# Kernel tuning notes

Hardware: AMD Instinct MI355X
Metric: run time of the kernel (lower is better)

Reference implementation:

```python
import jax, jax.numpy as jnp
import numpy as np
import math

TAU = 3.0
THRESHOLD = 0.25
BETA = 10.0
DT = 1.0


def setup_inputs() -> dict:
    key = jax.random.key(0)
    B, F, L = 64, 512, 1024
    I = jax.random.normal(key, (B, F, L), dtype=jnp.float32)
    return {"I": I}


def reference(I):
    dtype = I.dtype
    alpha = jnp.asarray(math.exp(-DT / TAU), dtype=dtype)
    thr = jnp.asarray(THRESHOLD, dtype=dtype)
    beta = jnp.asarray(BETA, dtype=dtype)

    B, F, L = I.shape
    I_t = jnp.moveaxis(I, -1, 0)  # (L, B, F) for scan over time
    v0 = jnp.zeros((B, F), dtype=dtype)

    def step(v, i_t):
        v_pre = alpha * v + (1 - alpha) * i_t
        z = beta * (v_pre - thr)
        s = (v_pre >= thr).astype(dtype)
        v_new = v_pre * (1 - s)  # threshold-triggered reset
        return v_new, (z, s)

    _, (z_hist, s_hist) = jax.lax.scan(step, v0, I_t)
    # (L, B, F) -> (B, F, L)
    return jnp.moveaxis(z_hist, 0, -1), jnp.moveaxis(s_hist, 0, -1)
```

## Files before the change

kernel.cpp:

```cpp
#include <hip/hip_runtime.h>


constexpr int L_LEN = 1024;

__global__ __launch_bounds__(64) void lif_kernel(
    const float* __restrict__ I, float* __restrict__ Z,
    float* __restrict__ S, int nrows)
{
#pragma clang fp contract(off)
    int row = blockIdx.x * 64 + threadIdx.x;
    if (row >= nrows) return;

    const float alpha = 0.7165313105737893f;
    const float oma   = 1.0f - alpha;
    const float thr   = 0.25f;
    const float beta  = 10.0f;

    const float4* in4 = reinterpret_cast<const float4*>(I) + (size_t)row * (L_LEN / 4);
    float4*       z4  = reinterpret_cast<float4*>(Z)       + (size_t)row * (L_LEN / 4);
    float4*       s4  = reinterpret_cast<float4*>(S)       + (size_t)row * (L_LEN / 4);

    float v = 0.0f;
#pragma unroll 8
    for (int t = 0; t < L_LEN / 4; ++t) {
        float4 x = in4[t];
        float4 zo, so;
        float vp;

        vp = alpha * v + oma * x.x;
        zo.x = beta * (vp - thr);
        so.x = (vp >= thr) ? 1.0f : 0.0f;
        v    = (vp >= thr) ? 0.0f : vp;

        vp = alpha * v + oma * x.y;
        zo.y = beta * (vp - thr);
        so.y = (vp >= thr) ? 1.0f : 0.0f;
        v    = (vp >= thr) ? 0.0f : vp;

        vp = alpha * v + oma * x.z;
        zo.z = beta * (vp - thr);
        so.z = (vp >= thr) ? 1.0f : 0.0f;
        v    = (vp >= thr) ? 0.0f : vp;

        vp = alpha * v + oma * x.w;
        zo.w = beta * (vp - thr);
        so.w = (vp >= thr) ? 1.0f : 0.0f;
        v    = (vp >= thr) ? 0.0f : vp;

        z4[t] = zo;
        s4[t] = so;
    }
}

extern "C" void kernel_launch(void* const* d_in, const int* in_sizes, int n_in,
                              void* d_out, int out_size, void* d_ws, size_t ws_size,
                              hipStream_t stream) {
    const float* I = (const float*)d_in[0];
    int n_elems = in_sizes[0];
    int nrows   = n_elems / L_LEN;

    float* Z = (float*)d_out;
    float* S = (float*)d_out + (size_t)n_elems;

    int block = 64;
    int grid  = (nrows + block - 1) / block;
    lif_kernel<<<grid, block, 0, stream>>>(I, Z, S, nrows);
}
```

Baseline: 424.0 us.

## Split LIF scan into state pass and chunk-parallel output pass

```diff
diff --git a/kernel.cpp b/kernel.cpp
--- a/kernel.cpp
+++ b/kernel.cpp
@@ -1,20 +1,119 @@
 #include <hip/hip_runtime.h>
 
 
-constexpr int L_LEN = 1024;
+constexpr int L_LEN  = 1024;
+constexpr int CHUNK  = 64;
+constexpr int NCHUNK = L_LEN / CHUNK;
 
-__global__ __launch_bounds__(64) void lif_kernel(
+#define ALPHA 0.7165313105737893f
+#define OMA   (1.0f - 0.7165313105737893f)
+#define THR   0.25f
+#define BETA  10.0f
+
+__global__ __launch_bounds__(64) void lif_phase1(
+    const float* __restrict__ I, float* __restrict__ states, int nrows)
+{
+#pragma clang fp contract(off)
+    int row = blockIdx.x * 64 + threadIdx.x;
+    if (row >= nrows) return;
+
+    const float4* in4 = reinterpret_cast<const float4*>(I) + (size_t)row * (L_LEN / 4);
+
+    float st[NCHUNK];
+    float v = 0.0f;
+
+    float4 buf[8];
+#pragma unroll
+    for (int j = 0; j < 8; ++j) buf[j] = in4[j];
+
+    const int nblk = L_LEN / 32;
+    for (int blk = 0; blk < nblk; ++blk) {
+        float4 nxt[8];
+        if (blk + 1 < nblk) {
+#pragma unroll
+            for (int j = 0; j < 8; ++j) nxt[j] = in4[(blk + 1) * 8 + j];
+        } else {
+#pragma unroll
+            for (int j = 0; j < 8; ++j) nxt[j] = make_float4(0.f, 0.f, 0.f, 0.f);
+        }
+
+        if ((blk & 1) == 0) st[blk >> 1] = v;
+
+#pragma unroll
+        for (int j = 0; j < 8; ++j) {
+            float4 x = buf[j];
+            float vp;
+            vp = ALPHA * v + OMA * x.x;  v = (vp >= THR) ? 0.0f : vp;
+            vp = ALPHA * v + OMA * x.y;  v = (vp >= THR) ? 0.0f : vp;
+            vp = ALPHA * v + OMA * x.z;  v = (vp >= THR) ? 0.0f : vp;
+            vp = ALPHA * v + OMA * x.w;  v = (vp >= THR) ? 0.0f : vp;
+        }
+#pragma unroll
+        for (int j = 0; j < 8; ++j) buf[j] = nxt[j];
+    }
+
+    float4* sp = reinterpret_cast<float4*>(states) + (size_t)row * (NCHUNK / 4);
+#pragma unroll
+    for (int c = 0; c < NCHUNK / 4; ++c)
+        sp[c] = make_float4(st[4*c], st[4*c+1], st[4*c+2], st[4*c+3]);
+}
+
+__global__ __launch_bounds__(256) void lif_phase2(
+    const float* __restrict__ I, const float* __restrict__ states,
+    float* __restrict__ Z, float* __restrict__ S, int nthreads)
+{
+#pragma clang fp contract(off)
+    int tid = blockIdx.x * 256 + threadIdx.x;
+    if (tid >= nthreads) return;
+
+    int row = tid >> 4;
+    int c   = tid & 15;
+
+    float v = states[tid];
+
+    size_t base = (size_t)row * (L_LEN / 4) + (size_t)c * (CHUNK / 4);
+    const float4* in4 = reinterpret_cast<const float4*>(I) + base;
+    float4*       z4  = reinterpret_cast<float4*>(Z) + base;
+    float4*       s4  = reinterpret_cast<float4*>(S) + base;
+
+#pragma unroll
+    for (int t = 0; t < CHUNK / 4; ++t) {
+        float4 x = in4[t];
+        float4 zo, so;
+        float vp;
+
+        vp = ALPHA * v + OMA * x.x;
+        zo.x = BETA * (vp - THR);
+        so.x = (vp >= THR) ? 1.0f : 0.0f;
+        v    = (vp >= THR) ? 0.0f : vp;
+
+        vp = ALPHA * v + OMA * x.y;
+        zo.y = BETA * (vp - THR);
+        so.y = (vp >= THR) ? 1.0f : 0.0f;
+        v    = (vp >= THR) ? 0.0f : vp;
+
+        vp = ALPHA * v + OMA * x.z;
+        zo.z = BETA * (vp - THR);
+        so.z = (vp >= THR) ? 1.0f : 0.0f;
+        v    = (vp >= THR) ? 0.0f : vp;
+
+        vp = ALPHA * v + OMA * x.w;
+        zo.w = BETA * (vp - THR);
+        so.w = (vp >= THR) ? 1.0f : 0.0f;
+        v    = (vp >= THR) ? 0.0f : vp;
+
+        z4[t] = zo;
+        s4[t] = so;
+    }
+}
+
+__global__ __launch_bounds__(64) void lif_single(
     const float* __restrict__ I, float* __restrict__ Z,
     float* __restrict__ S, int nrows)
 {
 #pragma clang fp contract(off)
     int row = blockIdx.x * 64 + threadIdx.x;
     if (row >= nrows) return;
-
-    const float alpha = 0.7165313105737893f;
-    const float oma   = 1.0f - alpha;
-    const float thr   = 0.25f;
-    const float beta  = 10.0f;
 
     const float4* in4 = reinterpret_cast<const float4*>(I) + (size_t)row * (L_LEN / 4);
     float4*       z4  = reinterpret_cast<float4*>(Z)       + (size_t)row * (L_LEN / 4);
@@ -26,27 +125,10 @@
         float4 x = in4[t];
         float4 zo, so;
         float vp;
-
-        vp = alpha * v + oma * x.x;
-        zo.x = beta * (vp - thr);
-        so.x = (vp >= thr) ? 1.0f : 0.0f;
-        v    = (vp >= thr) ? 0.0f : vp;
-
-        vp = alpha * v + oma * x.y;
-        zo.y = beta * (vp - thr);
-        so.y = (vp >= thr) ? 1.0f : 0.0f;
-        v    = (vp >= thr) ? 0.0f : vp;
-
-        vp = alpha * v + oma * x.z;
-        zo.z = beta * (vp - thr);
-        so.z = (vp >= thr) ? 1.0f : 0.0f;
-        v    = (vp >= thr) ? 0.0f : vp;
-
-        vp = alpha * v + oma * x.w;
-        zo.w = beta * (vp - thr);
-        so.w = (vp >= thr) ? 1.0f : 0.0f;
-        v    = (vp >= thr) ? 0.0f : vp;
-
+        vp = ALPHA * v + OMA * x.x; zo.x = BETA*(vp-THR); so.x = (vp>=THR)?1.f:0.f; v = (vp>=THR)?0.f:vp;
+        vp = ALPHA * v + OMA * x.y; zo.y = BETA*(vp-THR); so.y = (vp>=THR)?1.f:0.f; v = (vp>=THR)?0.f:vp;
+        vp = ALPHA * v + OMA * x.z; zo.z = BETA*(vp-THR); so.z = (vp>=THR)?1.f:0.f; v = (vp>=THR)?0.f:vp;
+        vp = ALPHA * v + OMA * x.w; zo.w = BETA*(vp-THR); so.w = (vp>=THR)?1.f:0.f; v = (vp>=THR)?0.f:vp;
         z4[t] = zo;
         s4[t] = so;
     }
@@ -62,7 +144,14 @@
     float* Z = (float*)d_out;
     float* S = (float*)d_out + (size_t)n_elems;
 
-    int block = 64;
-    int grid  = (nrows + block - 1) / block;
-    lif_kernel<<<grid, block, 0, stream>>>(I, Z, S, nrows);
+    size_t states_bytes = (size_t)nrows * NCHUNK * sizeof(float);
+
+    if (ws_size >= states_bytes) {
+        float* states = (float*)d_ws;
+        lif_phase1<<<(nrows + 63) / 64, 64, 0, stream>>>(I, states, nrows);
+        int nthreads = nrows * NCHUNK;
+        lif_phase2<<<(nthreads + 255) / 256, 256, 0, stream>>>(I, states, Z, S, nthreads);
+    } else {
+        lif_single<<<(nrows + 63) / 64, 64, 0, stream>>>(I, Z, S, nrows);
+    }
 }
```

Result: slower. 587.7 us (+38.6%).
